# Kernel optimization log

Measured on AMD Instinct MI355X. Metric: run time of the kernel, lower is better.

## Reference

```python
import math
import jax, jax.numpy as jnp
import numpy as np

EMBED_DIM = 512
NUM_HEADS = 8
PROJ_DIM = EMBED_DIM // NUM_HEADS
ATTN_WINDOW = 5
HALF_WINDOW = (ATTN_WINDOW - 1) // 2  # 2
ATTN_PARAM = 1.0
ATTN_DISPLACEMENT = 1
# per-head positions: ['center','left','right','center'] repeated to 8 heads (synst repeats short lists)
HEAD_SHIFTS = np.array([0, -ATTN_DISPLACEMENT, ATTN_DISPLACEMENT, 0] * 2, dtype=np.int32)


def _xavier(key, shape):
    fan_in, fan_out = shape[1], shape[0]
    bound = math.sqrt(6.0 / (fan_in + fan_out))
    return jax.random.uniform(key, shape, jnp.float32, -bound, bound)


def setup_inputs() -> dict:
    key = jax.random.key(0)
    k1, k2, k3, k4, k5 = jax.random.split(key, 5)
    B, S, E = 8, 4096, EMBED_DIM
    return {
        "values": jax.random.normal(k1, (B, S, E), jnp.float32),
        "keys": jax.random.normal(k2, (B, S, E), jnp.float32),
        "queries": jax.random.normal(k3, (B, S, E), jnp.float32),
        "input_weights": _xavier(k4, (E, E)),        # value projection (attn_weights=1, non-learned type)
        "out_proj_w": _xavier(k5, (E, E)),           # output_projection.weight (bias=False)
    }


def reference(values, keys, queries, input_weights, out_proj_w):
    # keys/queries are unused by the hard-coded 'normal' attention path (no QK^T)
    B, S, E = values.shape
    H, Dh, hw, W = NUM_HEADS, PROJ_DIM, HALF_WINDOW, ATTN_WINDOW

    # value projection + head split: [B,S,E] -> [B,H,S,Dh]
    v = values @ input_weights.T
    v = v.reshape(B, S, H, Dh).transpose(0, 2, 1, 3)

    # fixed Gaussian filter over relative distances [-hw, hw] (unnormalized pdf, as in the source)
    dist = jnp.arange(-hw, hw + 1, dtype=jnp.float32)
    filt = (1.0 / (ATTN_PARAM * math.sqrt(2.0 * math.pi))) * jnp.exp(-0.5 * (dist / ATTN_PARAM) ** 2)  # [W]

    shifts = jnp.asarray(HEAD_SHIFTS)            # [H] per-head center displacement
    P = hw + int(np.max(np.abs(HEAD_SHIFTS)))    # pad so all gathers are in range
    vp = jnp.pad(v, ((0, 0), (0, 0), (P, P), (0, 0)))  # [B,H,S+2P,Dh]

    h_ar = jnp.arange(H)[:, None]                # [H,1]
    pos = jnp.arange(S)[None, :]                 # [1,S]
    out = jnp.zeros_like(v)
    for j in range(W):                           # tiny fixed window loop (W=5)
        idx = pos + P + shifts[:, None] + (j - hw)   # [H,S]
        out = out + filt[j] * vp[:, h_ar, idx, :]    # [B,H,S,Dh]

    out = out.transpose(0, 2, 1, 3).reshape(B, S, E)
    return out @ out_proj_w.T
```

## Files before the change

### kernel.cpp

```cpp
#include <hip/hip_runtime.h>
#include <hip/hip_bf16.h>
#include <stdint.h>

typedef __bf16 bf16;
typedef __bf16 bf16x8 __attribute__((ext_vector_type(8)));
typedef float  f32x4  __attribute__((ext_vector_type(4)));

#define BM 128
#define BN 128
#define BK 32

__device__ __forceinline__ void gl_lds_16(const bf16* g, bf16* l) {
    __builtin_amdgcn_global_load_lds(
        (__attribute__((address_space(1))) void*)g,
        (__attribute__((address_space(3))) void*)l,
        16, 0, 0);
}

template<int OUT_BF16>
__global__ __launch_bounds__(256)
void gemm_bt(const bf16* __restrict__ A, const bf16* __restrict__ Bm,
             bf16* __restrict__ Cb, float* __restrict__ Cf,
             int M, int N, int K)
{
    __shared__ bf16 As[BM * BK];
    __shared__ bf16 Bs[BN * BK];

    const int tid  = threadIdx.x;
    const int bm   = blockIdx.x;
    const int bn   = blockIdx.y;
    const int wave = tid >> 6;
    const int lane = tid & 63;
    const int wm   = wave >> 1;
    const int wn   = wave & 1;

    const int srow = tid >> 2;
    const int scol = (tid & 3) << 3;
    const size_t a_off = (size_t)(bm * BM + srow) * K + scol;
    const size_t b_off = (size_t)(bn * BN + srow) * K + scol;
    const int    l_off = srow * BK + scol;

    f32x4 acc[4][4] = {};

    const int fr = lane & 15;
    const int ks = (lane >> 4) << 3;

    for (int k0 = 0; k0 < K; k0 += BK) {
        gl_lds_16(A  + a_off + k0,                 As + l_off);
        gl_lds_16(A  + a_off + (size_t)64 * K + k0, As + l_off + 64 * BK);
        gl_lds_16(Bm + b_off + k0,                 Bs + l_off);
        gl_lds_16(Bm + b_off + (size_t)64 * K + k0, Bs + l_off + 64 * BK);
        __syncthreads();

        bf16x8 af[4], bfr[4];
#pragma unroll
        for (int i = 0; i < 4; ++i) {
            af[i]  = *(const bf16x8*)(As + (wm * 64 + i * 16 + fr) * BK + ks);
            bfr[i] = *(const bf16x8*)(Bs + (wn * 64 + i * 16 + fr) * BK + ks);
        }
#pragma unroll
        for (int i = 0; i < 4; ++i)
#pragma unroll
            for (int j = 0; j < 4; ++j)
                acc[i][j] = __builtin_amdgcn_mfma_f32_16x16x32_bf16(af[i], bfr[j], acc[i][j], 0, 0, 0);
        __syncthreads();
    }

    const int crow = (lane >> 4) << 2;
    const int ccol = lane & 15;
    const int row0 = bm * BM + wm * 64 + crow;
    const int col0 = bn * BN + wn * 64 + ccol;
#pragma unroll
    for (int i = 0; i < 4; ++i)
#pragma unroll
        for (int j = 0; j < 4; ++j)
#pragma unroll
            for (int r = 0; r < 4; ++r) {
                size_t idx = (size_t)(row0 + i * 16 + r) * N + (col0 + j * 16);
                if (OUT_BF16) Cb[idx] = (bf16)acc[i][j][r];
                else          Cf[idx] = acc[i][j][r];
            }
}

__global__ __launch_bounds__(256)
void cvt_f32_bf16(const float* __restrict__ in, bf16* __restrict__ out, int n8)
{
    int i = blockIdx.x * 256 + threadIdx.x;
    if (i >= n8) return;
    const f32x4* p = (const f32x4*)in + 2 * (size_t)i;
    f32x4 a = p[0], b = p[1];
    bf16x8 o;
    o[0] = (bf16)a[0]; o[1] = (bf16)a[1]; o[2] = (bf16)a[2]; o[3] = (bf16)a[3];
    o[4] = (bf16)b[0]; o[5] = (bf16)b[1]; o[6] = (bf16)b[2]; o[7] = (bf16)b[3];
    *((bf16x8*)out + i) = o;
}

__global__ __launch_bounds__(256)
void gauss_filter(const bf16* __restrict__ v, bf16* __restrict__ o)
{
    const int idx = blockIdx.x * 256 + threadIdx.x;
    const int e8  = idx & 63;
    const int m   = idx >> 6;
    const int s   = m & 4095;
    const int bb  = m >> 12;
    const int h   = e8 >> 3;
    const int hm  = h & 3;
    const int sh  = (hm == 1) ? -1 : ((hm == 2) ? 1 : 0);

    const float filt[5] = {0.05399096651318806f, 0.24197072451914337f,
                           0.3989422804014327f,
                           0.24197072451914337f, 0.05399096651318806f};
    float acc[8] = {0.f, 0.f, 0.f, 0.f, 0.f, 0.f, 0.f, 0.f};
#pragma unroll
    for (int j = 0; j < 5; ++j) {
        int sp = s + sh + j - 2;
        if (sp >= 0 && sp < 4096) {
            bf16x8 x = *((const bf16x8*)(v + ((size_t)(bb * 4096 + sp)) * 512) + e8);
            float w = filt[j];
#pragma unroll
            for (int d = 0; d < 8; ++d) acc[d] += w * (float)x[d];
        }
    }
    bf16x8 r;
#pragma unroll
    for (int d = 0; d < 8; ++d) r[d] = (bf16)acc[d];
    *((bf16x8*)o + idx) = r;
}

extern "C" void kernel_launch(void* const* d_in, const int* in_sizes, int n_in,
                              void* d_out, int out_size, void* d_ws, size_t ws_size,
                              hipStream_t stream)
{
    const float* values = (const float*)d_in[0];
    const float* w_in   = (const float*)d_in[3];
    const float* w_out  = (const float*)d_in[4];
    float* out = (float*)d_out;

    const int Mrows = 8 * 4096;
    const int E = 512;

    bf16* win_b  = (bf16*)d_ws;
    bf16* wout_b = win_b + 512 * 512;
    bf16* vfilt  = wout_b + 512 * 512;

    bf16* vals_b = (bf16*)d_out;
    bf16* v_b    = vals_b + (size_t)Mrows * E;

    cvt_f32_bf16<<<(Mrows * E / 8 + 255) / 256, 256, 0, stream>>>(values, vals_b, Mrows * E / 8);
    cvt_f32_bf16<<<(E * E / 8 + 255) / 256, 256, 0, stream>>>(w_in,  win_b,  E * E / 8);
    cvt_f32_bf16<<<(E * E / 8 + 255) / 256, 256, 0, stream>>>(w_out, wout_b, E * E / 8);

    dim3 g1(Mrows / BM, E / BN);
    gemm_bt<1><<<g1, 256, 0, stream>>>(vals_b, win_b, v_b, nullptr, Mrows, E, E);

    gauss_filter<<<Mrows * 64 / 256, 256, 0, stream>>>(v_b, vfilt);

    gemm_bt<0><<<g1, 256, 0, stream>>>(vfilt, wout_b, nullptr, out, Mrows, E, E);
}
```

Before: 260.7 us.

## Apply Gaussian filter on fp32 inputs before projection, gather shifts in second GEMM

Because the Gaussian filter is linear along the sequence axis, it commutes with the value projection. The filter now runs once on the raw fp32 values, which also does the bf16 conversion, producing a padded per-batch buffer. The per-head shift is moved into the output GEMM's A-tile loads as a row offset. This removes the separate full-size fp32 to bf16 conversion pass and the filter pass over projected values, and merges the two weight conversions into one launch. The cost is a slightly larger first GEMM from the padded rows, plus rounding to bf16 at a different point.

```diff
diff --git a/kernel.cpp b/kernel.cpp
--- a/kernel.cpp
+++ b/kernel.cpp
@@ -9,6 +9,10 @@
 #define BM 128
 #define BN 128
 #define BK 32
+#define E  512
+#define SB 4112
+#define M1 (8 * SB)
+#define M2 32768
 
 __device__ __forceinline__ void gl_lds_16(const bf16* g, bf16* l) {
     __builtin_amdgcn_global_load_lds(
@@ -17,11 +21,9 @@
         16, 0, 0);
 }
 
-template<int OUT_BF16>
-__global__ __launch_bounds__(256)
-void gemm_bt(const bf16* __restrict__ A, const bf16* __restrict__ Bm,
-             bf16* __restrict__ Cb, float* __restrict__ Cf,
-             int M, int N, int K)
+__global__ __launch_bounds__(256)
+void gemm_bt_bf16(const bf16* __restrict__ A, const bf16* __restrict__ Bm,
+                  bf16* __restrict__ C, int M, int N, int K)
 {
     __shared__ bf16 As[BM * BK];
     __shared__ bf16 Bs[BN * BK];
@@ -41,14 +43,13 @@
     const int    l_off = srow * BK + scol;
 
     f32x4 acc[4][4] = {};
-
     const int fr = lane & 15;
     const int ks = (lane >> 4) << 3;
 
     for (int k0 = 0; k0 < K; k0 += BK) {
-        gl_lds_16(A  + a_off + k0,                 As + l_off);
+        gl_lds_16(A  + a_off + k0,                  As + l_off);
         gl_lds_16(A  + a_off + (size_t)64 * K + k0, As + l_off + 64 * BK);
-        gl_lds_16(Bm + b_off + k0,                 Bs + l_off);
+        gl_lds_16(Bm + b_off + k0,                  Bs + l_off);
         gl_lds_16(Bm + b_off + (size_t)64 * K + k0, Bs + l_off + 64 * BK);
         __syncthreads();
 
@@ -75,56 +76,125 @@
 #pragma unroll
         for (int j = 0; j < 4; ++j)
 #pragma unroll
-            for (int r = 0; r < 4; ++r) {
-                size_t idx = (size_t)(row0 + i * 16 + r) * N + (col0 + j * 16);
-                if (OUT_BF16) Cb[idx] = (bf16)acc[i][j][r];
-                else          Cf[idx] = acc[i][j][r];
-            }
-}
-
-__global__ __launch_bounds__(256)
-void cvt_f32_bf16(const float* __restrict__ in, bf16* __restrict__ out, int n8)
-{
-    int i = blockIdx.x * 256 + threadIdx.x;
-    if (i >= n8) return;
-    const f32x4* p = (const f32x4*)in + 2 * (size_t)i;
-    f32x4 a = p[0], b = p[1];
-    bf16x8 o;
-    o[0] = (bf16)a[0]; o[1] = (bf16)a[1]; o[2] = (bf16)a[2]; o[3] = (bf16)a[3];
-    o[4] = (bf16)b[0]; o[5] = (bf16)b[1]; o[6] = (bf16)b[2]; o[7] = (bf16)b[3];
-    *((bf16x8*)out + i) = o;
-}
-
-__global__ __launch_bounds__(256)
-void gauss_filter(const bf16* __restrict__ v, bf16* __restrict__ o)
+            for (int r = 0; r < 4; ++r)
+                C[(size_t)(row0 + i * 16 + r) * N + (col0 + j * 16)] = (bf16)acc[i][j][r];
+}
+
+__global__ __launch_bounds__(256)
+void gemm2_gather(const bf16* __restrict__ P, const bf16* __restrict__ Bm,
+                  float* __restrict__ C)
+{
+    __shared__ bf16 As[BM * BK];
+    __shared__ bf16 Bs[BN * BK];
+
+    const int tid  = threadIdx.x;
+    const int bm   = blockIdx.x;
+    const int bn   = blockIdx.y;
+    const int wave = tid >> 6;
+    const int lane = tid & 63;
+    const int wm   = wave >> 1;
+    const int wn   = wave & 1;
+
+    const int srow = tid >> 2;
+    const int scol = (tid & 3) << 3;
+
+    const int m0 = bm * BM + srow;
+    const int m1 = m0 + 64;
+    const int prow0 = (m0 >> 12) * SB + (m0 & 4095) + 1;
+    const int prow1 = (m1 >> 12) * SB + (m1 & 4095) + 1;
+
+    const size_t b_off = (size_t)(bn * BN + srow) * E + scol;
+    const int    l_off = srow * BK + scol;
+
+    f32x4 acc[4][4] = {};
+    const int fr = lane & 15;
+    const int ks = (lane >> 4) << 3;
+
+    for (int k0 = 0; k0 < E; k0 += BK) {
+        const int h3 = (k0 >> 6) & 3;
+        const int sh = (h3 == 1) ? -1 : (h3 == 2) ? 1 : 0;
+        gl_lds_16(P + (size_t)(prow0 + sh) * E + scol + k0, As + l_off);
+        gl_lds_16(P + (size_t)(prow1 + sh) * E + scol + k0, As + l_off + 64 * BK);
+        gl_lds_16(Bm + b_off + k0,                          Bs + l_off);
+        gl_lds_16(Bm + b_off + (size_t)64 * E + k0,         Bs + l_off + 64 * BK);
+        __syncthreads();
+
+        bf16x8 af[4], bfr[4];
+#pragma unroll
+        for (int i = 0; i < 4; ++i) {
+            af[i]  = *(const bf16x8*)(As + (wm * 64 + i * 16 + fr) * BK + ks);
+            bfr[i] = *(const bf16x8*)(Bs + (wn * 64 + i * 16 + fr) * BK + ks);
+        }
+#pragma unroll
+        for (int i = 0; i < 4; ++i)
+#pragma unroll
+            for (int j = 0; j < 4; ++j)
+                acc[i][j] = __builtin_amdgcn_mfma_f32_16x16x32_bf16(af[i], bfr[j], acc[i][j], 0, 0, 0);
+        __syncthreads();
+    }
+
+    const int crow = (lane >> 4) << 2;
+    const int ccol = lane & 15;
+    const int row0 = bm * BM + wm * 64 + crow;
+    const int col0 = bn * BN + wn * 64 + ccol;
+#pragma unroll
+    for (int i = 0; i < 4; ++i)
+#pragma unroll
+        for (int j = 0; j < 4; ++j)
+#pragma unroll
+            for (int r = 0; r < 4; ++r)
+                C[(size_t)(row0 + i * 16 + r) * E + (col0 + j * 16)] = acc[i][j][r];
+}
+
+__global__ __launch_bounds__(256)
+void prefilter(const float* __restrict__ vals, bf16* __restrict__ vg)
 {
     const int idx = blockIdx.x * 256 + threadIdx.x;
     const int e8  = idx & 63;
     const int m   = idx >> 6;
-    const int s   = m & 4095;
-    const int bb  = m >> 12;
-    const int h   = e8 >> 3;
-    const int hm  = h & 3;
-    const int sh  = (hm == 1) ? -1 : ((hm == 2) ? 1 : 0);
+    const int b   = m / SB;
+    const int r   = m - b * SB;
 
     const float filt[5] = {0.05399096651318806f, 0.24197072451914337f,
                            0.3989422804014327f,
                            0.24197072451914337f, 0.05399096651318806f};
     float acc[8] = {0.f, 0.f, 0.f, 0.f, 0.f, 0.f, 0.f, 0.f};
-#pragma unroll
-    for (int j = 0; j < 5; ++j) {
-        int sp = s + sh + j - 2;
-        if (sp >= 0 && sp < 4096) {
-            bf16x8 x = *((const bf16x8*)(v + ((size_t)(bb * 4096 + sp)) * 512) + e8);
-            float w = filt[j];
-#pragma unroll
-            for (int d = 0; d < 8; ++d) acc[d] += w * (float)x[d];
+    if (r < 4098) {
+#pragma unroll
+        for (int j = 0; j < 5; ++j) {
+            const int sp = r - 3 + j;
+            if (sp >= 0 && sp < 4096) {
+                const f32x4* p = (const f32x4*)(vals + ((size_t)(b * 4096 + sp)) * E + e8 * 8);
+                f32x4 x0 = p[0], x1 = p[1];
+                const float w = filt[j];
+                acc[0] += w * x0[0]; acc[1] += w * x0[1];
+                acc[2] += w * x0[2]; acc[3] += w * x0[3];
+                acc[4] += w * x1[0]; acc[5] += w * x1[1];
+                acc[6] += w * x1[2]; acc[7] += w * x1[3];
+            }
         }
     }
-    bf16x8 r;
-#pragma unroll
-    for (int d = 0; d < 8; ++d) r[d] = (bf16)acc[d];
-    *((bf16x8*)o + idx) = r;
+    bf16x8 o;
+#pragma unroll
+    for (int d = 0; d < 8; ++d) o[d] = (bf16)acc[d];
+    *((bf16x8*)vg + idx) = o;
+}
+
+__global__ __launch_bounds__(256)
+void cvt_weights(const float* __restrict__ w_in, const float* __restrict__ w_out,
+                 bf16* __restrict__ win_b, bf16* __restrict__ wout_b)
+{
+    const int i = blockIdx.x * 256 + threadIdx.x;
+    const int half = (E * E) / 8;
+    const float* src = (i < half) ? w_in : w_out;
+    bf16* dst        = (i < half) ? win_b : wout_b;
+    const int k = (i < half) ? i : i - half;
+    const f32x4* p = (const f32x4*)src + 2 * (size_t)k;
+    f32x4 a = p[0], bq = p[1];
+    bf16x8 o;
+    o[0] = (bf16)a[0]; o[1] = (bf16)a[1]; o[2] = (bf16)a[2]; o[3] = (bf16)a[3];
+    o[4] = (bf16)bq[0]; o[5] = (bf16)bq[1]; o[6] = (bf16)bq[2]; o[7] = (bf16)bq[3];
+    *((bf16x8*)dst + k) = o;
 }
 
 extern "C" void kernel_launch(void* const* d_in, const int* in_sizes, int n_in,
@@ -136,24 +206,17 @@
     const float* w_out  = (const float*)d_in[4];
     float* out = (float*)d_out;
 
-    const int Mrows = 8 * 4096;
-    const int E = 512;
-
     bf16* win_b  = (bf16*)d_ws;
-    bf16* wout_b = win_b + 512 * 512;
-    bf16* vfilt  = wout_b + 512 * 512;
-
-    bf16* vals_b = (bf16*)d_out;
-    bf16* v_b    = vals_b + (size_t)Mrows * E;
-
-    cvt_f32_bf16<<<(Mrows * E / 8 + 255) / 256, 256, 0, stream>>>(values, vals_b, Mrows * E / 8);
-    cvt_f32_bf16<<<(E * E / 8 + 255) / 256, 256, 0, stream>>>(w_in,  win_b,  E * E / 8);
-    cvt_f32_bf16<<<(E * E / 8 + 255) / 256, 256, 0, stream>>>(w_out, wout_b, E * E / 8);
-
-    dim3 g1(Mrows / BM, E / BN);
-    gemm_bt<1><<<g1, 256, 0, stream>>>(vals_b, win_b, v_b, nullptr, Mrows, E, E);
-
-    gauss_filter<<<Mrows * 64 / 256, 256, 0, stream>>>(v_b, vfilt);
-
-    gemm_bt<0><<<g1, 256, 0, stream>>>(vfilt, wout_b, nullptr, out, Mrows, E, E);
-}
+    bf16* wout_b = win_b + E * E;
+    bf16* vg     = wout_b + E * E;
+    bf16* Pbuf   = vg + (size_t)M1 * E;
+
+    cvt_weights<<<(2 * E * E / 8) / 256, 256, 0, stream>>>(w_in, w_out, win_b, wout_b);
+    prefilter<<<(size_t)M1 * 64 / 256, 256, 0, stream>>>(values, vg);
+
+    dim3 g1(M1 / BM, E / BN);
+    gemm_bt_bf16<<<g1, 256, 0, stream>>>(vg, win_b, Pbuf, M1, E, E);
+
+    dim3 g2(M2 / BM, E / BN);
+    gemm2_gather<<<g2, 256, 0, stream>>>(Pbuf, wout_b, out);
+}
```

Result: no change. 257.1 us (-1.4%).
